# Performance work log

Hardware: AMD Instinct MI355X
Metric: run time of the kernel (lower is better)

## Reference

```python
import jax, jax.numpy as jnp
import numpy as np

# dims
N, E, B, T = 1024, 8192, 4, 8          # nodes, edges, batch, time steps
IN, HID, H, NCLASS = 64, 64, 4, 7      # in_dim, nhidden, heads, nclass
K = N - NCLASS + 1                     # output-head conv width
NEG, EPS = 0.2, 1e-5


def setup_inputs() -> dict:
    key = jax.random.key(0)
    ks = jax.random.split(key, 24)
    p = lambda i, shape: jax.random.normal(ks[i], shape, jnp.float32) * 0.05
    inputs = jax.random.normal(ks[0], (B, IN, T, N), jnp.float32)
    src = jax.random.randint(ks[1], (E,), 0, N, jnp.int32)
    dst = jnp.repeat(jnp.arange(N, dtype=jnp.int32), E // N)  # every node has in-degree 8
    return {
        "inputs": inputs, "src": src, "dst": dst,
        "W0": p(2, (H * HID, IN)), "al0": p(3, (H, HID)), "ar0": p(4, (H, HID)),
        "W1": p(5, (H * HID, H * HID)), "al1": p(6, (H, HID)), "ar1": p(7, (H, HID)),
        "W2": p(8, (H * 1, H * HID)), "al2": p(9, (H, 1)), "ar2": p(10, (H, 1)),
        "Wres2": p(11, (H * 1, H * HID)),
        # Outputlayer
        "tc1_w": p(12, (H, H, T)), "tc1_b": p(13, (H,)),
        "ln1_g": jnp.ones((N, H), jnp.float32), "ln1_b": jnp.zeros((N, H), jnp.float32),
        "tc2_w": p(14, (1, H)), "tc2_b": p(15, (1,)),
        "ln2_g": jnp.ones((N, 1), jnp.float32), "ln2_b": jnp.zeros((N, 1), jnp.float32),
        "fc_w": p(16, (K,)), "fc_b": p(17, (1,)),
    }


def _gat_conv(h, src, dst, W, al, ar, res=None, act=None):
    # h: (N,B,T,F) -> feat: (N,B,T,H,D)
    heads, d = al.shape
    feat = (h @ W.T).reshape(N, B, T, heads, d)
    el = jnp.einsum('nbthd,hd->nbth', feat, al)
    er = jnp.einsum('nbthd,hd->nbth', feat, ar)
    e = jax.nn.leaky_relu(el[src] + er[dst], NEG)           # (E,B,T,H)
    emax = jax.ops.segment_max(e, dst, num_segments=N)
    ex = jnp.exp(e - emax[dst])
    den = jax.ops.segment_sum(ex, dst, num_segments=N)
    a = ex / den[dst]                                        # edge softmax over incoming edges
    out = jax.ops.segment_sum(feat[src] * a[..., None], dst, num_segments=N)  # (N,B,T,H,D)
    if res is not None:
        out = out + res
    if act is not None:
        out = act(out)
    return out


def reference(inputs, src, dst,
              W0, al0, ar0, W1, al1, ar1, W2, al2, ar2, Wres2,
              tc1_w, tc1_b, ln1_g, ln1_b, tc2_w, tc2_b, ln2_g, ln2_b, fc_w, fc_b):
    # (B,IN,T,N) -> (N,B,T,IN) : transpose(0,3).transpose(1,3)
    h = jnp.transpose(inputs.astype(jnp.float32), (3, 0, 2, 1))
    h1 = _gat_conv(h, src, dst, W0, al0, ar0, act=jax.nn.elu).reshape(N, B, T, H * HID)
    h2 = _gat_conv(h1, src, dst, W1, al1, ar1,
                   res=h1.reshape(N, B, T, H, HID), act=jax.nn.elu).reshape(N, B, T, H * HID)
    res2 = (h2 @ Wres2.T).reshape(N, B, T, H, 1)
    o = _gat_conv(h2, src, dst, W2, al2, ar2, res=res2)      # (N,B,T,H,1)
    # transpose(1,3).transpose(0,3).squeeze(-1) -> (B,H,T,N)
    x = jnp.transpose(o[..., 0], (1, 3, 2, 0))

    # Outputlayer
    # tconv1: Conv2d(H->H, kernel (T,1)) collapses time -> (B,H,N)
    x1 = jnp.einsum('oht,bhtn->bon', tc1_w, x) + tc1_b[None, :, None]
    # ln1: LayerNorm over (N,H) of (B,1,N,H)
    z = jnp.transpose(x1, (0, 2, 1))                          # (B,N,H)
    mu = z.mean(axis=(1, 2), keepdims=True)
    var = z.var(axis=(1, 2), keepdims=True)
    z = (z - mu) / jnp.sqrt(var + EPS) * ln1_g + ln1_b
    x1 = jnp.transpose(z, (0, 2, 1))                          # (B,H,N)
    # tconv2: 1x1 conv H->1 -> (B,1,N)
    x2 = jnp.einsum('oh,bhn->bon', tc2_w, x1) + tc2_b[None, :, None]
    # ln2: LayerNorm over (N,1)
    mu = x2.mean(axis=2, keepdims=True)
    var = x2.var(axis=2, keepdims=True)
    x2 = (x2 - mu) / jnp.sqrt(var + EPS) * ln2_g[:, 0] + ln2_b[:, 0]
    # fc: Conv2d(1->1, kernel (1,K)) sliding over nodes -> (B,NCLASS)
    xc = x2[:, :, None, :]                                    # (B,1,1,N) NCHW
    w = fc_w[None, None, None, :]                             # (1,1,1,K) OIHW
    out = jax.lax.conv_general_dilated(xc, w, (1, 1), 'VALID') + fc_b[None, :, None, None]
    return out[:, 0, 0, :]                                    # (B, NCLASS)
```

## Files before the change

### kernel.cpp

```cpp
#include <hip/hip_runtime.h>
#include <math.h>

#define NEGS 0.2f
#define EPSF 1e-5f

typedef short s16x8 __attribute__((ext_vector_type(8)));
typedef float f32x4 __attribute__((ext_vector_type(4)));

__device__ __forceinline__ float b2f(unsigned short u) {
  union { unsigned int i; float f; } v; v.i = ((unsigned int)u) << 16; return v.f;
}
__device__ __forceinline__ unsigned short f2b(float f) {
  union { float f; unsigned int i; } v; v.f = f;
  unsigned int x = v.i;
  return (unsigned short)((x + 0x7fffu + ((x >> 16) & 1u)) >> 16);
}

__device__ __forceinline__ float block_reduce1024(float v, float* red) {
  #pragma unroll
  for (int o = 32; o > 0; o >>= 1) v += __shfl_down(v, o);
  __syncthreads();
  if ((threadIdx.x & 63) == 0) red[threadIdx.x >> 6] = v;
  __syncthreads();
  float s = 0.f;
  #pragma unroll
  for (int i = 0; i < 16; ++i) s += red[i];
  return s;
}

__global__ __launch_bounds__(256) void k_feat0(
    const float* __restrict__ inp, const float* __restrict__ W0,
    const float* __restrict__ W1, const float* __restrict__ al,
    const float* __restrict__ ar, unsigned short* __restrict__ feat,
    float* __restrict__ el, float* __restrict__ er,
    unsigned short* __restrict__ W1b)
{
  const int tid = threadIdx.x;
  if (blockIdx.x >= 512) {
    const int j = (blockIdx.x - 512) * 256 + tid;
    float4 w4 = *(const float4*)&W1[j*4];
    ushort4 o4; o4.x=f2b(w4.x); o4.y=f2b(w4.y); o4.z=f2b(w4.z); o4.w=f2b(w4.w);
    *(ushort4*)&W1b[j*4] = o4;
    return;
  }
  __shared__ __align__(16) unsigned short At[64][72];
  __shared__ __align__(16) unsigned short Lb[64*256];
  const int bt = blockIdx.x & 31;
  const int n0 = (blockIdx.x >> 5) * 64;
  const int b  = bt >> 3, t = bt & 7;
  const int w    = tid >> 6;
  const int lane = tid & 63;
  const int n16  = lane & 15;
  const int q    = lane >> 4;
  s16x8 bf[2][4];
  #pragma unroll
  for (int kc = 0; kc < 2; ++kc)
    #pragma unroll
    for (int ct = 0; ct < 4; ++ct) {
      const float* p = &W0[(size_t)((w*4 + ct)*16 + n16)*64 + kc*32 + q*8];
      float4 wa = *(const float4*)p;
      float4 wb = *(const float4*)(p + 4);
      s16x8 o;
      o[0]=(short)f2b(wa.x); o[1]=(short)f2b(wa.y); o[2]=(short)f2b(wa.z); o[3]=(short)f2b(wa.w);
      o[4]=(short)f2b(wb.x); o[5]=(short)f2b(wb.y); o[6]=(short)f2b(wb.z); o[7]=(short)f2b(wb.w);
      bf[kc][ct] = o;
    }
  {
    const int nn = tid & 63, cg = tid >> 6;
    #pragma unroll
    for (int c2 = 0; c2 < 8; ++c2) {
      int ch = (cg*8 + c2) * 2;
      float vx = inp[((size_t)(b*64 + ch  )*8 + t)*1024 + n0 + nn];
      float vy = inp[((size_t)(b*64 + ch+1)*8 + t)*1024 + n0 + nn];
      unsigned int pk = ((unsigned int)f2b(vy) << 16) | (unsigned int)f2b(vx);
      *(unsigned int*)&At[nn][ch] = pk;
    }
  }
  __syncthreads();
  f32x4 acc[4][4];
  #pragma unroll
  for (int rt = 0; rt < 4; ++rt)
    #pragma unroll
    for (int ct = 0; ct < 4; ++ct) acc[rt][ct] = (f32x4){0.f,0.f,0.f,0.f};
  #pragma unroll
  for (int kc = 0; kc < 2; ++kc) {
    s16x8 af[4];
    #pragma unroll
    for (int rt = 0; rt < 4; ++rt)
      af[rt] = *(const s16x8*)&At[rt*16 + n16][kc*32 + q*8];
    #pragma unroll
    for (int rt = 0; rt < 4; ++rt)
      #pragma unroll
      for (int ct = 0; ct < 4; ++ct)
        acc[rt][ct] = __builtin_amdgcn_mfma_f32_16x16x32_bf16(af[rt], bf[kc][ct], acc[rt][ct], 0, 0, 0);
  }
  float alv[4], arv[4];
  #pragma unroll
  for (int ct = 0; ct < 4; ++ct) {
    alv[ct] = al[w*64 + ct*16 + n16];
    arv[ct] = ar[w*64 + ct*16 + n16];
  }
  #pragma unroll
  for (int rt = 0; rt < 4; ++rt) {
    #pragma unroll
    for (int reg = 0; reg < 4; ++reg) {
      float pl = acc[rt][0][reg]*alv[0] + acc[rt][1][reg]*alv[1]
               + acc[rt][2][reg]*alv[2] + acc[rt][3][reg]*alv[3];
      float pr = acc[rt][0][reg]*arv[0] + acc[rt][1][reg]*arv[1]
               + acc[rt][2][reg]*arv[2] + acc[rt][3][reg]*arv[3];
      #pragma unroll
      for (int o = 1; o < 16; o <<= 1) { pl += __shfl_xor(pl, o); pr += __shfl_xor(pr, o); }
      if (n16 == 0) {
        int r = (n0 + rt*16 + q*4 + reg)*32 + bt;
        el[r*4 + w] = pl;
        er[r*4 + w] = pr;
      }
    }
  }
  #pragma unroll
  for (int rt = 0; rt < 4; ++rt)
    #pragma unroll
    for (int ct = 0; ct < 4; ++ct)
      #pragma unroll
      for (int reg = 0; reg < 4; ++reg)
        Lb[(rt*16 + q*4 + reg)*256 + w*64 + ct*16 + n16] = f2b(acc[rt][ct][reg]);
  __syncthreads();
  #pragma unroll
  for (int i = 0; i < 8; ++i) {
    int u = tid + i*256;
    int m = u >> 5, off = (u & 31) * 8;
    *(s16x8*)&feat[(size_t)((n0 + m)*32 + bt)*256 + off] = *(const s16x8*)&Lb[m*256 + off];
  }
}

__global__ __launch_bounds__(256, 4) void k_agg0_feat1(
    const unsigned short* __restrict__ feat0, const float* __restrict__ el0,
    const float* __restrict__ er0, const int* __restrict__ src,
    const unsigned short* __restrict__ W1b, const float* __restrict__ al,
    const float* __restrict__ ar, unsigned short* __restrict__ h1b,
    unsigned short* __restrict__ feat1, float* __restrict__ el1, float* __restrict__ er1)
{
  __shared__ float wsm[8][32][4];
  __shared__ int   ssm[8];
  __shared__ __align__(16) unsigned short smbuf[32*264];
  unsigned short (*At)[264] = (unsigned short(*)[264])smbuf;
  unsigned short *Lb = smbuf;
  const int tid = threadIdx.x;
  const int n   = blockIdx.x;
  if (tid < 8) ssm[tid] = src[n*8 + tid];
  __syncthreads();
  if (tid < 128) {
    const int m = tid >> 2, h = tid & 3;
    const int rn = n*32 + m;
    const float erv = er0[rn*4 + h];
    float e[8]; float mx = -1e30f;
    #pragma unroll
    for (int j = 0; j < 8; ++j) {
      float v = el0[(ssm[j]*32 + m)*4 + h] + erv;
      v = v >= 0.f ? v : NEGS * v;
      e[j] = v; mx = fmaxf(mx, v);
    }
    float den = 0.f;
    #pragma unroll
    for (int j = 0; j < 8; ++j) { e[j] = __expf(e[j] - mx); den += e[j]; }
    const float inv = 1.f / den;
    #pragma unroll
    for (int j = 0; j < 8; ++j) wsm[j][m][h] = e[j] * inv;
  }
  __syncthreads();
  {
    const int hw2 = tid >> 5, l5 = tid & 31;
    const int c0 = l5 * 8, hh = l5 >> 3;
    #pragma unroll
    for (int p2 = 0; p2 < 2; ++p2) {
      const int mA = p2*16 + hw2, mB = mA + 8;
      s16x8 vA[8], vB[8];
      #pragma unroll
      for (int j = 0; j < 8; ++j) {
        vA[j] = *(const s16x8*)&feat0[(size_t)(ssm[j]*32 + mA)*256 + c0];
        vB[j] = *(const s16x8*)&feat0[(size_t)(ssm[j]*32 + mB)*256 + c0];
      }
      asm volatile("" ::: "memory");
      float aA[8] = {0,0,0,0,0,0,0,0}, aB[8] = {0,0,0,0,0,0,0,0};
      #pragma unroll
      for (int j = 0; j < 8; ++j) {
        const float wA = wsm[j][mA][hh], wB = wsm[j][mB][hh];
        #pragma unroll
        for (int i = 0; i < 8; ++i) {
          aA[i] = fmaf(wA, b2f((unsigned short)vA[j][i]), aA[i]);
          aB[i] = fmaf(wB, b2f((unsigned short)vB[j][i]), aB[i]);
        }
      }
      s16x8 oA, oB;
      #pragma unroll
      for (int i = 0; i < 8; ++i) {
        float xA = aA[i] > 0.f ? aA[i] : expm1f(aA[i]);
        float xB = aB[i] > 0.f ? aB[i] : expm1f(aB[i]);
        oA[i] = (short)f2b(xA); oB[i] = (short)f2b(xB);
      }
      *(s16x8*)&At[mA][c0] = oA;
      *(s16x8*)&At[mB][c0] = oB;
      *(s16x8*)&h1b[(size_t)(n*32 + mA)*256 + c0] = oA;
      *(s16x8*)&h1b[(size_t)(n*32 + mB)*256 + c0] = oB;
    }
  }
  __syncthreads();
  const int w    = tid >> 6;
  const int lane = tid & 63;
  const int n16  = lane & 15;
  const int q    = lane >> 4;
  const int r0   = n * 32;
  f32x4 acc[2][4];
  #pragma unroll
  for (int rt = 0; rt < 2; ++rt)
    #pragma unroll
    for (int ct = 0; ct < 4; ++ct) acc[rt][ct] = (f32x4){0.f,0.f,0.f,0.f};
  #pragma unroll
  for (int kc = 0; kc < 8; ++kc) {
    s16x8 af[2], bfr[4];
    #pragma unroll
    for (int rt = 0; rt < 2; ++rt)
      af[rt] = *(const s16x8*)&At[rt*16 + n16][kc*32 + q*8];
    #pragma unroll
    for (int ct = 0; ct < 4; ++ct)
      bfr[ct] = *(const s16x8*)&W1b[(size_t)((w*4 + ct)*16 + n16)*256 + kc*32 + q*8];
    #pragma unroll
    for (int rt = 0; rt < 2; ++rt)
      #pragma unroll
      for (int ct = 0; ct < 4; ++ct)
        acc[rt][ct] = __builtin_amdgcn_mfma_f32_16x16x32_bf16(af[rt], bfr[ct], acc[rt][ct], 0, 0, 0);
  }
  float alv[4], arv[4];
  #pragma unroll
  for (int ct = 0; ct < 4; ++ct) {
    alv[ct] = al[w*64 + ct*16 + n16];
    arv[ct] = ar[w*64 + ct*16 + n16];
  }
  #pragma unroll
  for (int rt = 0; rt < 2; ++rt) {
    #pragma unroll
    for (int reg = 0; reg < 4; ++reg) {
      float pl = acc[rt][0][reg]*alv[0] + acc[rt][1][reg]*alv[1]
               + acc[rt][2][reg]*alv[2] + acc[rt][3][reg]*alv[3];
      float pr = acc[rt][0][reg]*arv[0] + acc[rt][1][reg]*arv[1]
               + acc[rt][2][reg]*arv[2] + acc[rt][3][reg]*arv[3];
      #pragma unroll
      for (int o = 1; o < 16; o <<= 1) { pl += __shfl_xor(pl, o); pr += __shfl_xor(pr, o); }
      if (n16 == 0) {
        int r = r0 + rt*16 + q*4 + reg;
        el1[r*4 + w] = pl;
        er1[r*4 + w] = pr;
      }
    }
  }
  __syncthreads();
  #pragma unroll
  for (int rt = 0; rt < 2; ++rt)
    #pragma unroll
    for (int ct = 0; ct < 4; ++ct)
      #pragma unroll
      for (int reg = 0; reg < 4; ++reg)
        Lb[(rt*16 + q*4 + reg)*256 + w*64 + ct*16 + n16] = f2b(acc[rt][ct][reg]);
  __syncthreads();
  #pragma unroll
  for (int i = 0; i < 4; ++i) {
    int u = tid + i*256;
    int row = u >> 5, off = (u & 31) * 8;
    *(s16x8*)&feat1[(size_t)(r0 + row)*256 + off] = *(const s16x8*)&Lb[row*256 + off];
  }
}

__global__ __launch_bounds__(256, 4) void k_agg1_proj(
    const unsigned short* __restrict__ feat1, const float* __restrict__ el,
    const float* __restrict__ er, const int* __restrict__ src,
    const unsigned short* __restrict__ h1b, const float* __restrict__ W2,
    const float* __restrict__ Wres2, float* __restrict__ feat2, float* __restrict__ res2)
{
  __shared__ float wsm[8][32][4];
  __shared__ int   ssm[8];
  __shared__ __align__(16) float Wp[8][256];
  const int tid = threadIdx.x;
  const int n   = blockIdx.x;
  if (tid < 8) ssm[tid] = src[n*8 + tid];
  for (int j2 = tid; j2 < 2048; j2 += 256) {
    int o = j2 >> 8, k = j2 & 255;
    Wp[o][k] = (o < 4) ? W2[o*256 + k] : Wres2[(o-4)*256 + k];
  }
  __syncthreads();
  if (tid < 128) {
    const int m = tid >> 2, h = tid & 3;
    const int rn = n*32 + m;
    const float erv = er[rn*4 + h];
    float e[8]; float mx = -1e30f;
    #pragma unroll
    for (int j = 0; j < 8; ++j) {
      float v = el[(ssm[j]*32 + m)*4 + h] + erv;
      v = v >= 0.f ? v : NEGS * v;
      e[j] = v; mx = fmaxf(mx, v);
    }
    float den = 0.f;
    #pragma unroll
    for (int j = 0; j < 8; ++j) { e[j] = __expf(e[j] - mx); den += e[j]; }
    const float inv = 1.f / den;
    #pragma unroll
    for (int j = 0; j < 8; ++j) wsm[j][m][h] = e[j] * inv;
  }
  __syncthreads();
  const int hw2 = tid >> 5, l5 = tid & 31;
  const int c0 = l5 * 8, hh = l5 >> 3;
  #pragma unroll
  for (int p2 = 0; p2 < 2; ++p2) {
    const int mA = p2*16 + hw2, mB = mA + 8;
    const int rnA = n*32 + mA, rnB = n*32 + mB;
    s16x8 vA[8], vB[8], rrA, rrB;
    rrA = *(const s16x8*)&h1b[(size_t)rnA*256 + c0];
    rrB = *(const s16x8*)&h1b[(size_t)rnB*256 + c0];
    #pragma unroll
    for (int j = 0; j < 8; ++j) {
      vA[j] = *(const s16x8*)&feat1[(size_t)(ssm[j]*32 + mA)*256 + c0];
      vB[j] = *(const s16x8*)&feat1[(size_t)(ssm[j]*32 + mB)*256 + c0];
    }
    asm volatile("" ::: "memory");
    float aA[8] = {0,0,0,0,0,0,0,0}, aB[8] = {0,0,0,0,0,0,0,0};
    #pragma unroll
    for (int j = 0; j < 8; ++j) {
      const float wA = wsm[j][mA][hh], wB = wsm[j][mB][hh];
      #pragma unroll
      for (int i = 0; i < 8; ++i) {
        aA[i] = fmaf(wA, b2f((unsigned short)vA[j][i]), aA[i]);
        aB[i] = fmaf(wB, b2f((unsigned short)vB[j][i]), aB[i]);
      }
    }
    #pragma unroll
    for (int i = 0; i < 8; ++i) {
      float xA = aA[i] + b2f((unsigned short)rrA[i]);
      float xB = aB[i] + b2f((unsigned short)rrB[i]);
      aA[i] = xA > 0.f ? xA : expm1f(xA);
      aB[i] = xB > 0.f ? xB : expm1f(xB);
    }
    #pragma unroll
    for (int o = 0; o < 8; ++o) {
      float4 wa = *(const float4*)&Wp[o][c0];
      float4 wb = *(const float4*)&Wp[o][c0 + 4];
      float pA = aA[0]*wa.x + aA[1]*wa.y + aA[2]*wa.z + aA[3]*wa.w
               + aA[4]*wb.x + aA[5]*wb.y + aA[6]*wb.z + aA[7]*wb.w;
      float pB = aB[0]*wa.x + aB[1]*wa.y + aB[2]*wa.z + aB[3]*wa.w
               + aB[4]*wb.x + aB[5]*wb.y + aB[6]*wb.z + aB[7]*wb.w;
      #pragma unroll
      for (int off = 1; off < 32; off <<= 1) {
        pA += __shfl_xor(pA, off);
        pB += __shfl_xor(pB, off);
      }
      if (l5 == 0) {
        if (o < 4) { feat2[rnA*4 + o] = pA; feat2[rnB*4 + o] = pB; }
        else       { res2[rnA*4 + (o-4)] = pA; res2[rnB*4 + (o-4)] = pB; }
      }
    }
  }
}

__global__ __launch_bounds__(128) void k_agg2(
    const float* __restrict__ feat2, const float* __restrict__ res2,
    const int* __restrict__ src, const float* __restrict__ al2,
    const float* __restrict__ ar2, const float* __restrict__ tc1w,
    const float* __restrict__ tc1b, float* __restrict__ x1)
{
  __shared__ float os[4][8][4];
  const int n = blockIdx.x;
  const int tid = threadIdx.x;
  const int b = tid >> 5, t = (tid >> 2) & 7, h = tid & 3;
  const int rn = n*32 + b*8 + t;
  const float av = al2[h], rv = ar2[h];
  const float erv = feat2[rn*4 + h] * rv;
  float f[8], e[8]; float m = -1e30f;
  #pragma unroll
  for (int j = 0; j < 8; ++j) {
    int s_ = src[n*8 + j];
    f[j] = feat2[(s_*32 + b*8 + t)*4 + h];
    float v = f[j]*av + erv;
    v = v >= 0.f ? v : NEGS * v;
    e[j] = v; m = fmaxf(m, v);
  }
  float den = 0.f, num = 0.f;
  #pragma unroll
  for (int j = 0; j < 8; ++j) { float ex = __expf(e[j]-m); den += ex; num = fmaf(ex, f[j], num); }
  os[b][t][h] = num/den + res2[rn*4 + h];
  __syncthreads();
  if (tid < 16) {
    int b2 = tid >> 2, o2 = tid & 3;
    float acc = tc1b[o2];
    #pragma unroll
    for (int hh = 0; hh < 4; ++hh)
      #pragma unroll
      for (int tt = 0; tt < 8; ++tt)
        acc = fmaf(tc1w[(o2*4 + hh)*8 + tt], os[b2][tt][hh], acc);
    x1[(b2*4 + o2)*1024 + n] = acc;
  }
}

__global__ __launch_bounds__(1024) void k_final(
    const float* __restrict__ x1, const float* __restrict__ ln1g,
    const float* __restrict__ ln1b, const float* __restrict__ tc2w,
    const float* __restrict__ tc2b, const float* __restrict__ ln2g,
    const float* __restrict__ ln2b, const float* __restrict__ fcw,
    const float* __restrict__ fcb, float* __restrict__ out)
{
  __shared__ float red[16];
  __shared__ float x2s[1024];
  const int b = blockIdx.x;
  const int tid = threadIdx.x;
  float s = 0.f, q = 0.f;
  for (int j = tid; j < 4096; j += 1024) {
    float v = x1[b*4096 + j];
    s += v; q += v*v;
  }
  float S = block_reduce1024(s, red);
  float Q = block_reduce1024(q, red);
  float mu  = S * (1.f/4096.f);
  float var = Q * (1.f/4096.f) - mu*mu;
  float inv = rsqrtf(var + EPSF);
  float tb = tc2b[0];
  const int nn = tid;
  float acc = tb;
  #pragma unroll
  for (int h = 0; h < 4; ++h) {
    float z = (x1[b*4096 + h*1024 + nn] - mu) * inv * ln1g[nn*4 + h] + ln1b[nn*4 + h];
    acc = fmaf(tc2w[h], z, acc);
  }
  float S2 = block_reduce1024(acc, red);
  float Q2 = block_reduce1024(acc*acc, red);
  float mu2  = S2 * (1.f/1024.f);
  float inv2 = rsqrtf(Q2 * (1.f/1024.f) - mu2*mu2 + EPSF);
  x2s[nn] = (acc - mu2) * inv2 * ln2g[nn] + ln2b[nn];
  __syncthreads();
  for (int c = 0; c < 7; ++c) {
    float p = (tid < 1018) ? x2s[c + tid] * fcw[tid] : 0.f;
    float P = block_reduce1024(p, red);
    if (tid == 0) out[b*7 + c] = P + fcb[0];
  }
}

extern "C" void kernel_launch(void* const* d_in, const int* in_sizes, int n_in,
                              void* d_out, int out_size, void* d_ws, size_t ws_size,
                              hipStream_t stream)
{
  const float* inp  = (const float*)d_in[0];
  const int*   src  = (const int*)  d_in[1];
  const float* W0   = (const float*)d_in[3];
  const float* al0  = (const float*)d_in[4];
  const float* ar0  = (const float*)d_in[5];
  const float* W1   = (const float*)d_in[6];
  const float* al1  = (const float*)d_in[7];
  const float* ar1  = (const float*)d_in[8];
  const float* W2   = (const float*)d_in[9];
  const float* al2  = (const float*)d_in[10];
  const float* ar2  = (const float*)d_in[11];
  const float* Wr2  = (const float*)d_in[12];
  const float* tc1w = (const float*)d_in[13];
  const float* tc1b = (const float*)d_in[14];
  const float* ln1g = (const float*)d_in[15];
  const float* ln1b = (const float*)d_in[16];
  const float* tc2w = (const float*)d_in[17];
  const float* tc2b = (const float*)d_in[18];
  const float* ln2g = (const float*)d_in[19];
  const float* ln2b = (const float*)d_in[20];
  const float* fcw  = (const float*)d_in[21];
  const float* fcb  = (const float*)d_in[22];
  float* out = (float*)d_out;

  unsigned short* W1b    = (unsigned short*)d_ws;
  unsigned short* featb0 = W1b    + 65536;
  unsigned short* featb1 = featb0 + 8388608;
  unsigned short* h1b    = featb1 + 8388608;
  float* el0   = (float*)(h1b + 8388608);
  float* er0   = el0   + 131072;
  float* el1   = er0   + 131072;
  float* er1   = el1   + 131072;
  float* feat2 = er1   + 131072;
  float* res2  = feat2 + 131072;
  float* x1    = res2  + 131072;

  k_feat0<<<dim3(576), dim3(256), 0, stream>>>(inp, W0, W1, al0, ar0,
                                               featb0, el0, er0, W1b);
  k_agg0_feat1<<<dim3(1024), dim3(256), 0, stream>>>(featb0, el0, er0, src, W1b, al1, ar1,
                                                     h1b, featb1, el1, er1);
  k_agg1_proj<<<dim3(1024), dim3(256), 0, stream>>>(featb1, el1, er1, src, h1b, W2, Wr2,
                                                    feat2, res2);
  k_agg2<<<dim3(1024), dim3(128), 0, stream>>>(feat2, res2, src, al2, ar2, tc1w, tc1b, x1);
  k_final<<<dim3(4), dim3(1024), 0, stream>>>(x1, ln1g, ln1b, tc2w, tc2b, ln2g, ln2b, fcw, fcb, out);
}
```

Before: 176.1 us.

## Remap aggregation blocks to 32 nodes per (b,t) slice with XCD-aware grouping

The aggregation kernels previously gave each block one node with all 32 (b,t) rows. Now each block handles 32 consecutive nodes at one fixed (b,t) slice, and the blockIdx-to-bt mapping is permuted so that the 8 blocks in a group (likely landing on different XCDs) take distinct bt groups. The intent is for blocks sharing a bt slice to be scheduled on the same XCD, so gathered neighbour rows of feat0/feat1 and el/er get reused in that XCD's L2 instead of being spread across all caches. The cost is that each gathered row read is now strided by 32 rows in memory, and the layer-1 feature rows written from a block are no longer contiguous.

Measured after the change: 170.7 us (median of 3 runs). -3.1%, faster.

```diff
diff --git a/kernel.cpp b/kernel.cpp
--- a/kernel.cpp
+++ b/kernel.cpp
@@ -45,7 +45,8 @@
   }
   __shared__ __align__(16) unsigned short At[64][72];
   __shared__ __align__(16) unsigned short Lb[64*256];
-  const int bt = blockIdx.x & 31;
+  const int g  = blockIdx.x & 7;
+  const int bt = g*4 + ((blockIdx.x >> 3) & 3);
   const int n0 = (blockIdx.x >> 5) * 64;
   const int b  = bt >> 3, t = bt & 7;
   const int w    = tid >> 6;
@@ -140,23 +141,25 @@
     const float* __restrict__ ar, unsigned short* __restrict__ h1b,
     unsigned short* __restrict__ feat1, float* __restrict__ el1, float* __restrict__ er1)
 {
-  __shared__ float wsm[8][32][4];
-  __shared__ int   ssm[8];
+  __shared__ float wsm[32][8][4];
+  __shared__ int   ssm[32][8];
   __shared__ __align__(16) unsigned short smbuf[32*264];
   unsigned short (*At)[264] = (unsigned short(*)[264])smbuf;
   unsigned short *Lb = smbuf;
   const int tid = threadIdx.x;
-  const int n   = blockIdx.x;
-  if (tid < 8) ssm[tid] = src[n*8 + tid];
+  const int g     = blockIdx.x & 7;
+  const int bt    = g*4 + ((blockIdx.x >> 3) & 3);
+  const int nBase = (blockIdx.x >> 5) * 32;
+  ((int*)ssm)[tid] = src[nBase*8 + tid];
   __syncthreads();
   if (tid < 128) {
-    const int m = tid >> 2, h = tid & 3;
-    const int rn = n*32 + m;
+    const int nl = tid >> 2, h = tid & 3;
+    const int rn = (nBase + nl)*32 + bt;
     const float erv = er0[rn*4 + h];
     float e[8]; float mx = -1e30f;
     #pragma unroll
     for (int j = 0; j < 8; ++j) {
-      float v = el0[(ssm[j]*32 + m)*4 + h] + erv;
+      float v = el0[(ssm[nl][j]*32 + bt)*4 + h] + erv;
       v = v >= 0.f ? v : NEGS * v;
       e[j] = v; mx = fmaxf(mx, v);
     }
@@ -165,7 +168,7 @@
     for (int j = 0; j < 8; ++j) { e[j] = __expf(e[j] - mx); den += e[j]; }
     const float inv = 1.f / den;
     #pragma unroll
-    for (int j = 0; j < 8; ++j) wsm[j][m][h] = e[j] * inv;
+    for (int j = 0; j < 8; ++j) wsm[nl][j][h] = e[j] * inv;
   }
   __syncthreads();
   {
@@ -173,18 +176,18 @@
     const int c0 = l5 * 8, hh = l5 >> 3;
     #pragma unroll
     for (int p2 = 0; p2 < 2; ++p2) {
-      const int mA = p2*16 + hw2, mB = mA + 8;
+      const int nlA = p2*16 + hw2, nlB = nlA + 8;
       s16x8 vA[8], vB[8];
       #pragma unroll
       for (int j = 0; j < 8; ++j) {
-        vA[j] = *(const s16x8*)&feat0[(size_t)(ssm[j]*32 + mA)*256 + c0];
-        vB[j] = *(const s16x8*)&feat0[(size_t)(ssm[j]*32 + mB)*256 + c0];
+        vA[j] = *(const s16x8*)&feat0[(size_t)(ssm[nlA][j]*32 + bt)*256 + c0];
+        vB[j] = *(const s16x8*)&feat0[(size_t)(ssm[nlB][j]*32 + bt)*256 + c0];
       }
       asm volatile("" ::: "memory");
       float aA[8] = {0,0,0,0,0,0,0,0}, aB[8] = {0,0,0,0,0,0,0,0};
       #pragma unroll
       for (int j = 0; j < 8; ++j) {
-        const float wA = wsm[j][mA][hh], wB = wsm[j][mB][hh];
+        const float wA = wsm[nlA][j][hh], wB = wsm[nlB][j][hh];
         #pragma unroll
         for (int i = 0; i < 8; ++i) {
           aA[i] = fmaf(wA, b2f((unsigned short)vA[j][i]), aA[i]);
@@ -198,10 +201,10 @@
         float xB = aB[i] > 0.f ? aB[i] : expm1f(aB[i]);
         oA[i] = (short)f2b(xA); oB[i] = (short)f2b(xB);
       }
-      *(s16x8*)&At[mA][c0] = oA;
-      *(s16x8*)&At[mB][c0] = oB;
-      *(s16x8*)&h1b[(size_t)(n*32 + mA)*256 + c0] = oA;
-      *(s16x8*)&h1b[(size_t)(n*32 + mB)*256 + c0] = oB;
+      *(s16x8*)&At[nlA][c0] = oA;
+      *(s16x8*)&At[nlB][c0] = oB;
+      *(s16x8*)&h1b[(size_t)((nBase + nlA)*32 + bt)*256 + c0] = oA;
+      *(s16x8*)&h1b[(size_t)((nBase + nlB)*32 + bt)*256 + c0] = oB;
     }
   }
   __syncthreads();
@@ -209,7 +212,6 @@
   const int lane = tid & 63;
   const int n16  = lane & 15;
   const int q    = lane >> 4;
-  const int r0   = n * 32;
   f32x4 acc[2][4];
   #pragma unroll
   for (int rt = 0; rt < 2; ++rt)
@@ -247,7 +249,7 @@
       #pragma unroll
       for (int o = 1; o < 16; o <<= 1) { pl += __shfl_xor(pl, o); pr += __shfl_xor(pr, o); }
       if (n16 == 0) {
-        int r = r0 + rt*16 + q*4 + reg;
+        int r = (nBase + rt*16 + q*4 + reg)*32 + bt;
         el1[r*4 + w] = pl;
         er1[r*4 + w] = pr;
       }
@@ -266,7 +268,7 @@
   for (int i = 0; i < 4; ++i) {
     int u = tid + i*256;
     int row = u >> 5, off = (u & 31) * 8;
-    *(s16x8*)&feat1[(size_t)(r0 + row)*256 + off] = *(const s16x8*)&Lb[row*256 + off];
+    *(s16x8*)&feat1[(size_t)((nBase + row)*32 + bt)*256 + off] = *(const s16x8*)&Lb[row*256 + off];
   }
 }
 
@@ -276,25 +278,27 @@
     const unsigned short* __restrict__ h1b, const float* __restrict__ W2,
     const float* __restrict__ Wres2, float* __restrict__ feat2, float* __restrict__ res2)
 {
-  __shared__ float wsm[8][32][4];
-  __shared__ int   ssm[8];
+  __shared__ float wsm[32][8][4];
+  __shared__ int   ssm[32][8];
   __shared__ __align__(16) float Wp[8][256];
   const int tid = threadIdx.x;
-  const int n   = blockIdx.x;
-  if (tid < 8) ssm[tid] = src[n*8 + tid];
+  const int g     = blockIdx.x & 7;
+  const int bt    = g*4 + ((blockIdx.x >> 3) & 3);
+  const int nBase = (blockIdx.x >> 5) * 32;
+  ((int*)ssm)[tid] = src[nBase*8 + tid];
   for (int j2 = tid; j2 < 2048; j2 += 256) {
     int o = j2 >> 8, k = j2 & 255;
     Wp[o][k] = (o < 4) ? W2[o*256 + k] : Wres2[(o-4)*256 + k];
   }
   __syncthreads();
   if (tid < 128) {
-    const int m = tid >> 2, h = tid & 3;
-    const int rn = n*32 + m;
+    const int nl = tid >> 2, h = tid & 3;
+    const int rn = (nBase + nl)*32 + bt;
     const float erv = er[rn*4 + h];
     float e[8]; float mx = -1e30f;
     #pragma unroll
     for (int j = 0; j < 8; ++j) {
-      float v = el[(ssm[j]*32 + m)*4 + h] + erv;
+      float v = el[(ssm[nl][j]*32 + bt)*4 + h] + erv;
       v = v >= 0.f ? v : NEGS * v;
       e[j] = v; mx = fmaxf(mx, v);
     }
@@ -303,28 +307,28 @@
     for (int j = 0; j < 8; ++j) { e[j] = __expf(e[j] - mx); den += e[j]; }
     const float inv = 1.f / den;
     #pragma unroll
-    for (int j = 0; j < 8; ++j) wsm[j][m][h] = e[j] * inv;
+    for (int j = 0; j < 8; ++j) wsm[nl][j][h] = e[j] * inv;
   }
   __syncthreads();
   const int hw2 = tid >> 5, l5 = tid & 31;
   const int c0 = l5 * 8, hh = l5 >> 3;
   #pragma unroll
   for (int p2 = 0; p2 < 2; ++p2) {
-    const int mA = p2*16 + hw2, mB = mA + 8;
-    const int rnA = n*32 + mA, rnB = n*32 + mB;
+    const int nlA = p2*16 + hw2, nlB = nlA + 8;
+    const int rnA = (nBase + nlA)*32 + bt, rnB = (nBase + nlB)*32 + bt;
     s16x8 vA[8], vB[8], rrA, rrB;
     rrA = *(const s16x8*)&h1b[(size_t)rnA*256 + c0];
     rrB = *(const s16x8*)&h1b[(size_t)rnB*256 + c0];
     #pragma unroll
     for (int j = 0; j < 8; ++j) {
-      vA[j] = *(const s16x8*)&feat1[(size_t)(ssm[j]*32 + mA)*256 + c0];
-      vB[j] = *(const s16x8*)&feat1[(size_t)(ssm[j]*32 + mB)*256 + c0];
+      vA[j] = *(const s16x8*)&feat1[(size_t)(ssm[nlA][j]*32 + bt)*256 + c0];
+      vB[j] = *(const s16x8*)&feat1[(size_t)(ssm[nlB][j]*32 + bt)*256 + c0];
     }
     asm volatile("" ::: "memory");
     float aA[8] = {0,0,0,0,0,0,0,0}, aB[8] = {0,0,0,0,0,0,0,0};
     #pragma unroll
     for (int j = 0; j < 8; ++j) {
-      const float wA = wsm[j][mA][hh], wB = wsm[j][mB][hh];
+      const float wA = wsm[nlA][j][hh], wB = wsm[nlB][j][hh];
       #pragma unroll
       for (int i = 0; i < 8; ++i) {
         aA[i] = fmaf(wA, b2f((unsigned short)vA[j][i]), aA[i]);
```
